# Kernel tuning notes

Hardware: AMD Instinct MI355X
Metric: run time of the kernel (lower is better)

Reference implementation:

```python
import jax, jax.numpy as jnp
import numpy as np

B, T, D_MODEL, HEAD_DIM = 4, 4096, 2048, 128
NEG = -1e9  # matches torch's -1000000000.0 mask fill


def setup_inputs() -> dict:
    key = jax.random.key(0)
    ks = jax.random.split(key, 7)
    s = 0.02
    return {
        "x": jax.random.normal(ks[0], (B, T, D_MODEL), dtype=jnp.float32),
        "q_w": jax.random.normal(ks[1], (HEAD_DIM, D_MODEL), dtype=jnp.float32) * s,
        "q_b": jax.random.normal(ks[2], (HEAD_DIM,), dtype=jnp.float32) * s,
        "k_w": jax.random.normal(ks[3], (HEAD_DIM, D_MODEL), dtype=jnp.float32) * s,
        "k_b": jax.random.normal(ks[4], (HEAD_DIM,), dtype=jnp.float32) * s,
        "v_w": jax.random.normal(ks[5], (HEAD_DIM, D_MODEL), dtype=jnp.float32) * s,
        "v_b": jax.random.normal(ks[6], (HEAD_DIM,), dtype=jnp.float32) * s,
    }


def reference(x, q_w, q_b, k_w, k_b, v_w, v_b):
    # Linear projections: y = x @ W^T + b  -> [B, T, head_dim]
    q = jnp.einsum("btc,hc->bth", x, q_w) + q_b
    k = jnp.einsum("btc,hc->bth", x, k_w) + k_b
    v = jnp.einsum("btc,hc->bth", x, v_w) + v_b

    head_dim = q.shape[-1]
    # scores [B, T, T], scaled by 1/sqrt(head_dim)
    scores = jnp.einsum("bqh,bkh->bqk", q, k) / jnp.sqrt(jnp.float32(head_dim))
    # causal mask: additive -1e9 above the diagonal (future positions)
    t = scores.shape[-1]
    mask = jnp.triu(jnp.full((t, t), NEG, dtype=scores.dtype), k=1)
    scores = scores + mask
    probs = jax.nn.softmax(scores, axis=-1)
    # dropout p=0.0 -> identity (eval)
    y = jnp.einsum("bqk,bkh->bqh", probs, v)
    return y
```

## Files before the change

### kernel.cpp

```cpp
#include <hip/hip_runtime.h>

#define T_SEQ 4096
#define DMODEL 2048
#define HD 128

typedef float f32x4 __attribute__((ext_vector_type(4)));
typedef _Float16 f16x8 __attribute__((ext_vector_type(8)));

__device__ __forceinline__ unsigned short f2h(float f) {
  union { _Float16 h; unsigned short u; } v;
  v.h = (_Float16)f;
  return v.u;
}

__device__ __forceinline__ unsigned pk2h(float lo, float hi) {
  return (unsigned)f2h(lo) | ((unsigned)f2h(hi) << 16);
}

__global__ __launch_bounds__(256) void cvt_w_kernel(
    const float* __restrict__ qw, const float* __restrict__ qb,
    const float* __restrict__ kw, const float* __restrict__ kb,
    const float* __restrict__ vw, const float* __restrict__ vb,
    unsigned short* __restrict__ wb, float* __restrict__ biasc) {
  int idx = blockIdx.x * 256 + threadIdx.x;
  int e = idx * 4;
  int row = e >> 11;
  int col = e & 2047;
  const float* src = (row < 128) ? (qw + row * 2048)
                   : (row < 256) ? (kw + (row - 128) * 2048)
                                 : (vw + (row - 256) * 2048);
  float4 v = *(const float4*)(src + col);
  ushort4 o;
  o.x = f2h(v.x); o.y = f2h(v.y); o.z = f2h(v.z); o.w = f2h(v.w);
  *(ushort4*)(wb + e) = o;
  if (blockIdx.x == 0 && threadIdx.x < 384) {
    int n = threadIdx.x;
    biasc[n] = (n < 128) ? qb[n] : (n < 256) ? kb[n - 128] : vb[n - 256];
  }
}

#define SAB 40
__global__ __launch_bounds__(256, 3) void proj_kernel(
    const float* __restrict__ x, const unsigned short* __restrict__ wb,
    const float* __restrict__ biasc, unsigned short* __restrict__ qkv) {
  __shared__ unsigned short sA[64 * SAB];
  __shared__ unsigned short sB[128 * SAB];
  const int tid = threadIdx.x;
  const int lane = tid & 63;
  const int w = tid >> 6;
  const int fr = lane & 15;
  const int g = lane >> 4;
  const int m0 = blockIdx.x * 64;
  const int n0 = blockIdx.y * 128;
  const int wm = (w & 1) * 32;
  const int wn = (w >> 1) * 64;

  const int arow = tid >> 2;
  const int acolA = (tid & 3) * 8;
  const int brow = tid >> 1;
  const int bcolB = (tid & 1) * 16;
  const float* xp = x + (size_t)(m0 + arow) * DMODEL + acolA;
  const unsigned short* bp = wb + (size_t)(n0 + brow) * DMODEL + bcolB;

  f32x4 acc[2][4] = {};
  float4 ax0 = *(const float4*)(xp);
  float4 ax1 = *(const float4*)(xp + 4);
  uint4 bx0 = *(const uint4*)(bp);
  uint4 bx1 = *(const uint4*)(bp + 8);

  for (int k0 = 0; k0 < DMODEL; k0 += 32) {
    __syncthreads();
    uint4 pa;
    pa.x = pk2h(ax0.x, ax0.y); pa.y = pk2h(ax0.z, ax0.w);
    pa.z = pk2h(ax1.x, ax1.y); pa.w = pk2h(ax1.z, ax1.w);
    *(uint4*)&sA[arow * SAB + acolA] = pa;
    *(uint4*)&sB[brow * SAB + bcolB] = bx0;
    *(uint4*)&sB[brow * SAB + bcolB + 8] = bx1;
    __syncthreads();

    if (k0 + 32 < DMODEL) {
      ax0 = *(const float4*)(xp + k0 + 32);
      ax1 = *(const float4*)(xp + k0 + 36);
      bx0 = *(const uint4*)(bp + k0 + 32);
      bx1 = *(const uint4*)(bp + k0 + 40);
    }

    f16x8 af[2], bf[4];
#pragma unroll
    for (int i = 0; i < 2; ++i)
      af[i] = *(const f16x8*)&sA[(wm + 16 * i + fr) * SAB + g * 8];
#pragma unroll
    for (int jn = 0; jn < 4; ++jn)
      bf[jn] = *(const f16x8*)&sB[(wn + 16 * jn + fr) * SAB + g * 8];
#pragma unroll
    for (int i = 0; i < 2; ++i)
#pragma unroll
      for (int jn = 0; jn < 4; ++jn)
        acc[i][jn] = __builtin_amdgcn_mfma_f32_16x16x32_f16(af[i], bf[jn], acc[i][jn], 0, 0, 0);
  }

#pragma unroll
  for (int jn = 0; jn < 4; ++jn) {
    int n = n0 + wn + 16 * jn + fr;
    float bias = biasc[n];
#pragma unroll
    for (int i = 0; i < 2; ++i) {
      int mb = m0 + wm + 16 * i + g * 4;
#pragma unroll
      for (int r = 0; r < 4; ++r)
        qkv[(size_t)(mb + r) * 384 + n] = f2h(acc[i][jn][r] + bias);
    }
  }
}

#define SKS 136
#define SVS 72
#define SPS 72
__global__ __launch_bounds__(256) void attn_kernel(
    const unsigned short* __restrict__ qkv, float* __restrict__ out,
    float* __restrict__ po, float* __restrict__ pml, int split) {
  __shared__ unsigned short sK[64 * SKS];
  __shared__ unsigned short sVt[128 * SVS];
  __shared__ unsigned short sP[64 * SPS];
  const int id = blockIdx.x;
  const int batch = blockIdx.y;
  int qt, c, nc;
  if (split) {
    if (id < 16)      { qt = id;                c = 0;          nc = 1; }
    else if (id < 48) { qt = 16 + ((id - 16) >> 1); c = (id - 16) & 1; nc = 2; }
    else if (id < 96) { qt = 32 + (id - 48) / 3;    c = (id - 48) % 3; nc = 3; }
    else              { qt = 48 + ((id - 96) >> 2); c = (id - 96) & 3; nc = 4; }
  } else { qt = id; c = 0; nc = 1; }
  const int qbase = qt * 64;
  const int t0 = c * 16;
  const int tend = min(t0 + 16, qt + 1);
  const int tid = threadIdx.x;
  const int lane = tid & 63;
  const int w = tid >> 6;
  const int fr = lane & 15;
  const int g = lane >> 4;
  const unsigned short* qkvb = qkv + (size_t)batch * T_SEQ * 384;

  f16x8 qf[4];
  {
    const unsigned short* qp = qkvb + (size_t)(qbase + 16 * w + fr) * 384 + g * 8;
#pragma unroll
    for (int s = 0; s < 4; ++s) qf[s] = *(const f16x8*)(qp + 32 * s);
  }
  f32x4 o[8] = {};
  float m_r[4], l_r[4];
#pragma unroll
  for (int r = 0; r < 4; ++r) { m_r[r] = -1e30f; l_r[r] = 0.f; }
  const float scale = 0.08838834764831845f;

  uint4 pk[4], pvv[4];
#pragma unroll
  for (int it = 0; it < 4; ++it) {
    int idx = it * 256 + tid;
    int row = idx >> 4;
    int u = idx & 15;
    const unsigned short* src = qkvb + (size_t)(t0 * 64 + row) * 384 + 128 + u * 8;
    pk[it] = *(const uint4*)src;
    pvv[it] = *(const uint4*)(src + 128);
  }

  for (int t = t0; t < tend; ++t) {
    const int kbase = t * 64;
    __syncthreads();
#pragma unroll
    for (int it = 0; it < 4; ++it) {
      int idx = it * 256 + tid;
      int row = idx >> 4;
      int u = idx & 15;
      int c8 = u * 8;
      *(uint4*)&sK[row * SKS + c8] = pk[it];
      unsigned short tv[8];
      *(uint4*)tv = pvv[it];
      int kidx = (row & 7) | (((row >> 3) ^ (u & 7)) << 3);
#pragma unroll
      for (int jj = 0; jj < 8; ++jj)
        sVt[(c8 + jj) * SVS + kidx] = tv[jj];
    }
    __syncthreads();

    if (t + 1 < tend) {
#pragma unroll
      for (int it = 0; it < 4; ++it) {
        int idx = it * 256 + tid;
        int row = idx >> 4;
        int u = idx & 15;
        const unsigned short* src = qkvb + (size_t)((t + 1) * 64 + row) * 384 + 128 + u * 8;
        pk[it] = *(const uint4*)src;
        pvv[it] = *(const uint4*)(src + 128);
      }
    }

    f32x4 sacc[4] = {};
#pragma unroll
    for (int ks = 0; ks < 4; ++ks)
#pragma unroll
      for (int tn = 0; tn < 4; ++tn) {
        f16x8 kf = *(const f16x8*)&sK[(16 * tn + fr) * SKS + 32 * ks + g * 8];
        sacc[tn] = __builtin_amdgcn_mfma_f32_16x16x32_f16(qf[ks], kf, sacc[tn], 0, 0, 0);
      }

    const bool diag = (t == qt);
    float pv[4][4];
#pragma unroll
    for (int r = 0; r < 4; ++r) {
      int grow = qbase + 16 * w + g * 4 + r;
      float mx = -1e30f;
#pragma unroll
      for (int tn = 0; tn < 4; ++tn) {
        float s = sacc[tn][r] * scale;
        if (diag && (kbase + 16 * tn + fr) > grow) s = -1e30f;
        pv[tn][r] = s;
        mx = fmaxf(mx, s);
      }
      mx = fmaxf(mx, __shfl_xor(mx, 1));
      mx = fmaxf(mx, __shfl_xor(mx, 2));
      mx = fmaxf(mx, __shfl_xor(mx, 4));
      mx = fmaxf(mx, __shfl_xor(mx, 8));
      float mnew = fmaxf(m_r[r], mx);
      float alpha = __expf(m_r[r] - mnew);
      m_r[r] = mnew;
      float rs = 0.f;
#pragma unroll
      for (int tn = 0; tn < 4; ++tn) {
        float p = __expf(pv[tn][r] - mnew);
        pv[tn][r] = p;
        rs += p;
      }
      rs += __shfl_xor(rs, 1);
      rs += __shfl_xor(rs, 2);
      rs += __shfl_xor(rs, 4);
      rs += __shfl_xor(rs, 8);
      l_r[r] = l_r[r] * alpha + rs;
#pragma unroll
      for (int nt = 0; nt < 8; ++nt) o[nt][r] *= alpha;
    }

#pragma unroll
    for (int tn = 0; tn < 4; ++tn)
#pragma unroll
      for (int r = 0; r < 4; ++r)
        sP[(w * 16 + g * 4 + r) * SPS + 16 * tn + fr] = f2h(pv[tn][r]);

#pragma unroll
    for (int ks = 0; ks < 2; ++ks) {
      f16x8 pa = *(const f16x8*)&sP[(w * 16 + fr) * SPS + 32 * ks + g * 8];
#pragma unroll
      for (int nt = 0; nt < 8; ++nt) {
        int d = 16 * nt + fr;
        int cc = (d >> 3) & 7;
        f16x8 vf = *(const f16x8*)&sVt[d * SVS + (((4 * ks + g) ^ cc) << 3)];
        o[nt] = __builtin_amdgcn_mfma_f32_16x16x32_f16(pa, vf, o[nt], 0, 0, 0);
      }
    }
  }

  if (nc == 1) {
#pragma unroll
    for (int r = 0; r < 4; ++r) {
      float inv = 1.0f / l_r[r];
      int grow = qbase + 16 * w + g * 4 + r;
      float* op = out + ((size_t)batch * T_SEQ + grow) * HD;
#pragma unroll
      for (int nt = 0; nt < 8; ++nt)
        op[16 * nt + fr] = o[nt][r] * inv;
    }
  } else {
    size_t slot = ((size_t)batch * 160 + id) * 64;
#pragma unroll
    for (int r = 0; r < 4; ++r) {
      int lrow = 16 * w + g * 4 + r;
      float* op = po + (slot + lrow) * 128;
#pragma unroll
      for (int nt = 0; nt < 8; ++nt)
        op[16 * nt + fr] = o[nt][r];
      if (fr == 0) {
        pml[(slot + lrow) * 2] = m_r[r];
        pml[(slot + lrow) * 2 + 1] = l_r[r];
      }
    }
  }
}

__global__ __launch_bounds__(256) void combine_kernel(
    const float* __restrict__ po, const float* __restrict__ pml,
    float* __restrict__ out) {
  int gr = blockIdx.x * 2 + (threadIdx.x >> 7);
  int d = threadIdx.x & 127;
  int batch = gr / 3072;
  int ridx = gr - batch * 3072;
  int qt = 16 + (ridx >> 6);
  int rr = ridx & 63;
  int nc = 1 + (qt >> 4);
  int sb = (qt < 32) ? 16 + (qt - 16) * 2
         : (qt < 48) ? 48 + (qt - 32) * 3
                     : 96 + (qt - 48) * 4;
  size_t base = ((size_t)batch * 160 + sb) * 64 + rr;
  float mi[4], li[4];
  float M = -1e30f;
#pragma unroll
  for (int i = 0; i < 4; ++i) {
    if (i < nc) {
      mi[i] = pml[(base + (size_t)i * 64) * 2];
      li[i] = pml[(base + (size_t)i * 64) * 2 + 1];
      M = fmaxf(M, mi[i]);
    }
  }
  float L = 0.f, acc = 0.f;
#pragma unroll
  for (int i = 0; i < 4; ++i) {
    if (i < nc) {
      float sc = __expf(mi[i] - M);
      L += li[i] * sc;
      acc += po[(base + (size_t)i * 64) * 128 + d] * sc;
    }
  }
  out[((size_t)batch * T_SEQ + qt * 64 + rr) * HD + d] = acc / L;
}

extern "C" void kernel_launch(void* const* d_in, const int* in_sizes, int n_in,
                              void* d_out, int out_size, void* d_ws, size_t ws_size,
                              hipStream_t stream) {
  const float* x  = (const float*)d_in[0];
  const float* qw = (const float*)d_in[1];
  const float* qb = (const float*)d_in[2];
  const float* kw = (const float*)d_in[3];
  const float* kb = (const float*)d_in[4];
  const float* vw = (const float*)d_in[5];
  const float* vb = (const float*)d_in[6];
  float* out = (float*)d_out;

  unsigned short* qkv = (unsigned short*)d_ws;
  unsigned short* wb  = qkv + (size_t)16384 * 384;
  float* biasc = (float*)(wb + (size_t)384 * 2048);
  float* po  = (float*)((char*)d_ws + 14157312);
  float* pml = po + (size_t)640 * 64 * 128;
  size_t need = 14157312 + (size_t)640 * 64 * 128 * 4 + (size_t)640 * 64 * 2 * 4;
  int split = (ws_size >= need) ? 1 : 0;

  cvt_w_kernel<<<768, 256, 0, stream>>>(qw, qb, kw, kb, vw, vb, wb, biasc);
  proj_kernel<<<dim3(256, 3), 256, 0, stream>>>(x, wb, biasc, qkv);
  attn_kernel<<<dim3(split ? 160 : 64, 4), 256, 0, stream>>>(qkv, out, po, pml, split);
  if (split)
    combine_kernel<<<6144, 256, 0, stream>>>(po, pml, out);
}
```

Baseline: 172.3 us.

## Vectorize V transpose via byte-perm, DPP reductions, packed P stores, occupancy hint

Reworks the V tile transpose into shared memory. Each thread now loads four rows of V and uses byte-permute to build 64-bit packed column stores, replacing eight scalar 16-bit stores per vector, with a new XOR swizzle that the PV-MFMA reads match. Row max and sum reductions use DPP lane moves instead of ds_swizzle shuffles. P is written as packed 64-bit stores with a permuted key order. The launch bound now requests three blocks per SIMD, which may cap registers and risk spills; the permuted P columns must stay consistent with the V layout for correctness.

```diff
diff --git a/kernel.cpp b/kernel.cpp
--- a/kernel.cpp
+++ b/kernel.cpp
@@ -15,6 +15,31 @@
 
 __device__ __forceinline__ unsigned pk2h(float lo, float hi) {
   return (unsigned)f2h(lo) | ((unsigned)f2h(hi) << 16);
+}
+
+template <int CTRL>
+__device__ __forceinline__ float dppmax(float x) {
+  union { float f; int i; } a, b;
+  a.f = x;
+  b.i = __builtin_amdgcn_update_dpp(a.i, a.i, CTRL, 0xF, 0xF, false);
+  return fmaxf(x, b.f);
+}
+template <int CTRL>
+__device__ __forceinline__ float dppadd(float x) {
+  union { float f; int i; } a, b;
+  a.f = x;
+  b.i = __builtin_amdgcn_update_dpp(a.i, a.i, CTRL, 0xF, 0xF, false);
+  return x + b.f;
+}
+__device__ __forceinline__ float red16_max(float x) {
+  x = dppmax<0xB1>(x); x = dppmax<0x4E>(x);
+  x = dppmax<0x124>(x); x = dppmax<0x128>(x);
+  return x;
+}
+__device__ __forceinline__ float red16_add(float x) {
+  x = dppadd<0xB1>(x); x = dppadd<0x4E>(x);
+  x = dppadd<0x124>(x); x = dppadd<0x128>(x);
+  return x;
 }
 
 __global__ __launch_bounds__(256) void cvt_w_kernel(
@@ -116,7 +141,7 @@
 #define SKS 136
 #define SVS 72
 #define SPS 72
-__global__ __launch_bounds__(256) void attn_kernel(
+__global__ __launch_bounds__(256, 3) void attn_kernel(
     const unsigned short* __restrict__ qkv, float* __restrict__ out,
     float* __restrict__ po, float* __restrict__ pml, int split) {
   __shared__ unsigned short sK[64 * SKS];
@@ -139,6 +164,9 @@
   const int w = tid >> 6;
   const int fr = lane & 15;
   const int g = lane >> 4;
+  const int va = tid >> 4;
+  const int vu = tid & 15;
+  const int vblk = ((va ^ (vu & 14)) << 2);
   const unsigned short* qkvb = qkv + (size_t)batch * T_SEQ * 384;
 
   f16x8 qf[4];
@@ -157,12 +185,11 @@
 #pragma unroll
   for (int it = 0; it < 4; ++it) {
     int idx = it * 256 + tid;
-    int row = idx >> 4;
-    int u = idx & 15;
-    const unsigned short* src = qkvb + (size_t)(t0 * 64 + row) * 384 + 128 + u * 8;
-    pk[it] = *(const uint4*)src;
-    pvv[it] = *(const uint4*)(src + 128);
-  }
+    pk[it] = *(const uint4*)(qkvb + (size_t)(t0 * 64 + (idx >> 4)) * 384 + 128 + (idx & 15) * 8);
+  }
+#pragma unroll
+  for (int i = 0; i < 4; ++i)
+    pvv[i] = *(const uint4*)(qkvb + (size_t)(t0 * 64 + va + 16 * i) * 384 + 256 + vu * 8);
 
   for (int t = t0; t < tend; ++t) {
     const int kbase = t * 64;
@@ -170,16 +197,23 @@
 #pragma unroll
     for (int it = 0; it < 4; ++it) {
       int idx = it * 256 + tid;
-      int row = idx >> 4;
-      int u = idx & 15;
-      int c8 = u * 8;
-      *(uint4*)&sK[row * SKS + c8] = pk[it];
-      unsigned short tv[8];
-      *(uint4*)tv = pvv[it];
-      int kidx = (row & 7) | (((row >> 3) ^ (u & 7)) << 3);
-#pragma unroll
-      for (int jj = 0; jj < 8; ++jj)
-        sVt[(c8 + jj) * SVS + kidx] = tv[jj];
+      *(uint4*)&sK[(idx >> 4) * SKS + (idx & 15) * 8] = pk[it];
+    }
+    {
+      const unsigned* w0 = (const unsigned*)&pvv[0];
+      const unsigned* w1 = (const unsigned*)&pvv[1];
+      const unsigned* w2 = (const unsigned*)&pvv[2];
+      const unsigned* w3 = (const unsigned*)&pvv[3];
+#pragma unroll
+      for (int j2 = 0; j2 < 4; ++j2) {
+        uint2 se, so;
+        se.x = __builtin_amdgcn_perm(w1[j2], w0[j2], 0x05040100);
+        se.y = __builtin_amdgcn_perm(w3[j2], w2[j2], 0x05040100);
+        so.x = __builtin_amdgcn_perm(w1[j2], w0[j2], 0x07060302);
+        so.y = __builtin_amdgcn_perm(w3[j2], w2[j2], 0x07060302);
+        *(uint2*)&sVt[(8 * vu + 2 * j2) * SVS + vblk] = se;
+        *(uint2*)&sVt[(8 * vu + 2 * j2 + 1) * SVS + vblk] = so;
+      }
     }
     __syncthreads();
 
@@ -187,12 +221,11 @@
 #pragma unroll
       for (int it = 0; it < 4; ++it) {
         int idx = it * 256 + tid;
-        int row = idx >> 4;
-        int u = idx & 15;
-        const unsigned short* src = qkvb + (size_t)((t + 1) * 64 + row) * 384 + 128 + u * 8;
-        pk[it] = *(const uint4*)src;
-        pvv[it] = *(const uint4*)(src + 128);
-      }
+        pk[it] = *(const uint4*)(qkvb + (size_t)((t + 1) * 64 + (idx >> 4)) * 384 + 128 + (idx & 15) * 8);
+      }
+#pragma unroll
+      for (int i = 0; i < 4; ++i)
+        pvv[i] = *(const uint4*)(qkvb + (size_t)((t + 1) * 64 + va + 16 * i) * 384 + 256 + vu * 8);
     }
 
     f32x4 sacc[4] = {};
@@ -217,10 +250,7 @@
         pv[tn][r] = s;
         mx = fmaxf(mx, s);
       }
-      mx = fmaxf(mx, __shfl_xor(mx, 1));
-      mx = fmaxf(mx, __shfl_xor(mx, 2));
-      mx = fmaxf(mx, __shfl_xor(mx, 4));
-      mx = fmaxf(mx, __shfl_xor(mx, 8));
+      mx = red16_max(mx);
       float mnew = fmaxf(m_r[r], mx);
       float alpha = __expf(m_r[r] - mnew);
       m_r[r] = mnew;
@@ -231,29 +261,28 @@
         pv[tn][r] = p;
         rs += p;
       }
-      rs += __shfl_xor(rs, 1);
-      rs += __shfl_xor(rs, 2);
-      rs += __shfl_xor(rs, 4);
-      rs += __shfl_xor(rs, 8);
+      rs = red16_add(rs);
       l_r[r] = l_r[r] * alpha + rs;
 #pragma unroll
       for (int nt = 0; nt < 8; ++nt) o[nt][r] *= alpha;
     }
 
 #pragma unroll
-    for (int tn = 0; tn < 4; ++tn)
-#pragma unroll
-      for (int r = 0; r < 4; ++r)
-        sP[(w * 16 + g * 4 + r) * SPS + 16 * tn + fr] = f2h(pv[tn][r]);
+    for (int r = 0; r < 4; ++r) {
+      uint2 pw;
+      pw.x = pk2h(pv[0][r], pv[1][r]);
+      pw.y = pk2h(pv[2][r], pv[3][r]);
+      *(uint2*)&sP[(16 * w + 4 * g + r) * SPS + 4 * fr] = pw;
+    }
 
 #pragma unroll
     for (int ks = 0; ks < 2; ++ks) {
-      f16x8 pa = *(const f16x8*)&sP[(w * 16 + fr) * SPS + 32 * ks + g * 8];
+      f16x8 pa = *(const f16x8*)&sP[(16 * w + fr) * SPS + 32 * ks + 8 * g];
 #pragma unroll
       for (int nt = 0; nt < 8; ++nt) {
         int d = 16 * nt + fr;
-        int cc = (d >> 3) & 7;
-        f16x8 vf = *(const f16x8*)&sVt[d * SVS + (((4 * ks + g) ^ cc) << 3)];
+        int blk = ((8 * ks + 2 * g) ^ ((d >> 3) & 14)) << 1;
+        f16x8 vf = *(const f16x8*)&sVt[d * SVS + (blk << 1)];
         o[nt] = __builtin_amdgcn_mfma_f32_16x16x32_f16(pa, vf, o[nt], 0, 0, 0);
       }
     }
```

Result: faster. 144.0 us (-16.5%).
